# Optimization experiments

Hardware: AMD Instinct MI355X
Metric: run time of the kernel (lower is better)

## Reference

```python
import jax, jax.numpy as jnp
import numpy as np

N = 8192        # points
M = 131072      # query-key pairs (edges)
C_IN = 512
H = 8           # heads
D = 64          # head_channels
BINS = 48
BIN_SIZE = 0.05


def setup_inputs() -> dict:
    key = jax.random.key(0)
    ks = jax.random.split(key, 8)
    x_F = jax.random.normal(ks[0], (N, C_IN), dtype=jnp.float32)
    x_C = jax.random.uniform(ks[1], (N, 3), dtype=jnp.float32)
    qk_pair_idxs = jax.random.randint(ks[2], (2, M), 0, N, dtype=jnp.int64)
    W_qkv = jax.random.normal(ks[3], (C_IN, 3 * H * D), dtype=jnp.float32) * 0.02
    b_qkv = jnp.zeros((3 * H * D,), dtype=jnp.float32)
    q_tables = jax.random.normal(ks[4], (3, BINS, H, D), dtype=jnp.float32) * 0.02
    k_tables = jax.random.normal(ks[5], (3, BINS, H, D), dtype=jnp.float32) * 0.02
    v_tables = jax.random.normal(ks[6], (3, BINS, H, D), dtype=jnp.float32) * 0.02
    return {"x_F": x_F, "x_C": x_C, "qk_pair_idxs": qk_pair_idxs,
            "W_qkv": W_qkv, "b_qkv": b_qkv,
            "q_tables": q_tables, "k_tables": k_tables, "v_tables": v_tables}


def reference(x_F, x_C, qk_pair_idxs, W_qkv, b_qkv, q_tables, k_tables, v_tables):
    n = x_F.shape[0]
    qkv = (x_F @ W_qkv + b_qkv).reshape(n, 3, H, D)
    q = qkv[:, 0] * (D ** -0.5)   # scale folded into queries, as in the module
    k = qkv[:, 1]
    v = qkv[:, 2]
    qi = qk_pair_idxs[0]
    ki = qk_pair_idxs[1]
    # quantized relative coordinates -> table bin indices [M,3]
    rel = (x_C[qi] - x_C[ki]) / BIN_SIZE + BINS / 2
    idx = jnp.clip(rel.astype(jnp.int32), 0, BINS - 1)
    # precompute per-point, per-axis, per-bin table dot products [N,3,BINS,H]
    q_dot = jnp.einsum('nhd,abhd->nabh', q, q_tables)
    k_dot = jnp.einsum('nhd,abhd->nabh', k, k_tables)
    # content logits [M,H]
    logits = jnp.einsum('mhd,mhd->mh', q[qi], k[ki])
    for a in range(3):  # fixed xyz axes
        logits = logits + q_dot[qi, a, idx[:, a]] + k_dot[ki, a, idx[:, a]]
    # scatter softmax over query index (per head)
    seg_max = jax.ops.segment_max(logits, qi, num_segments=n)
    e = jnp.exp(logits - seg_max[qi])
    denom = jax.ops.segment_sum(e, qi, num_segments=n)
    attn = e / denom[qi]  # [M,H]
    # value-side relative position bias, summed over axes [M,H,D]
    vt = v_tables[0, idx[:, 0]] + v_tables[1, idx[:, 1]] + v_tables[2, idx[:, 2]]
    contrib = attn[:, :, None] * (v[ki] + vt)            # [M,H,D]
    agg = jax.ops.segment_sum(contrib, qi, num_segments=n)  # [N,H,D]
    return agg.reshape(n, H * D)
```

## Files before the change

### kernel.cpp

```cpp
#include <hip/hip_runtime.h>
#include <hip/hip_bf16.h>
#include <stdint.h>

#define N_PTS 8192
#define M_EDGES 131072
#define CIN 512
#define QKV_COLS 1536

typedef __bf16 bf16x8 __attribute__((ext_vector_type(8)));
typedef float f32x4 __attribute__((ext_vector_type(4)));

#define GAS __attribute__((address_space(1)))
#define LAS __attribute__((address_space(3)))

__device__ __forceinline__ void gload_lds16(const void* g, void* l) {
  __builtin_amdgcn_global_load_lds((const GAS void*)g, (LAS void*)l, 16, 0, 0);
}

__global__ __launch_bounds__(256) void prep_kernel(
    const float* __restrict__ xF, const float* __restrict__ W,
    const float* __restrict__ qt, const float* __restrict__ kt,
    const float* __restrict__ vt, const int* __restrict__ pairs,
    const float* __restrict__ xc,
    __bf16* __restrict__ A, __bf16* __restrict__ BT,
    __bf16* __restrict__ qtb, __bf16* __restrict__ ktb, __bf16* __restrict__ vtb,
    int* __restrict__ qi_a, unsigned* __restrict__ pack0, int* __restrict__ cnt) {
  __shared__ float tile[32][33];
  int b = blockIdx.x;
  int tid = threadIdx.x;
  if (b < 4096) {
    int base = (b * 256 + tid) * 4;
    float4 v = *(const float4*)(xF + base);
    A[base + 0] = (__bf16)v.x;
    A[base + 1] = (__bf16)v.y;
    A[base + 2] = (__bf16)v.z;
    A[base + 3] = (__bf16)v.w;
  } else if (b < 4864) {
    int blk = b - 4096;
    int bk = blk & 15, bn = blk >> 4;
    int x = tid & 31, y = tid >> 5;
#pragma unroll
    for (int j = 0; j < 4; j++) {
      int r = y + j * 8;
      tile[r][x] = W[(size_t)(bk * 32 + r) * QKV_COLS + bn * 32 + x];
    }
    __syncthreads();
#pragma unroll
    for (int j = 0; j < 4; j++) {
      int r = y + j * 8;
      BT[(size_t)(bn * 32 + r) * CIN + bk * 32 + x] = (__bf16)tile[x][r];
    }
  } else if (b < 5152) {
    int i = (b - 4864) * 256 + tid;
    int d = i & 63, h = (i >> 6) & 7, ab = i >> 9;
    int po = (h * 144 + ab) * 64 + d;
    qtb[po] = (__bf16)qt[i];
    ktb[po] = (__bf16)kt[i];
    vtb[i] = (__bf16)vt[i];
  } else {
    int m = (b - 5152) * 256 + tid;
    int qi = pairs[m], ki = pairs[M_EDGES + m];
    unsigned pb = 0;
#pragma unroll
    for (int a = 0; a < 3; a++) {
      float rel = (xc[qi * 3 + a] - xc[ki * 3 + a]) / 0.05f + 24.0f;
      int bb = (int)rel;
      bb = bb < 0 ? 0 : (bb > 47 ? 47 : bb);
      pb |= (unsigned)bb << (6 * a);
    }
    qi_a[m] = qi;
    pack0[m] = (unsigned)ki | (pb << 13);
    atomicAdd(&cnt[qi], 1);
  }
}

__global__ __launch_bounds__(256) void gemm_qkv(const __bf16* __restrict__ A,
                                                const __bf16* __restrict__ BT,
                                                const float* __restrict__ bias,
                                                __bf16* __restrict__ qb,
                                                __bf16* __restrict__ kb,
                                                __bf16* __restrict__ vb) {
  __shared__ __align__(16) char At[128 * 128];
  __shared__ __align__(16) char Bt[128 * 128];
  int tid = threadIdx.x;
  int w = tid >> 6, l = tid & 63;
  int bm = blockIdx.x, bn = blockIdx.y;
  int wm = w & 1, wn = w >> 1;
  f32x4 acc[4][4] = {};
  const char* Ab = (const char*)A;
  const char* Bb = (const char*)BT;
  int lr = l & 15;
  int lk = (l >> 4) * 16;
  int xr = (lr & 7) << 4;

  for (int kt = 0; kt < 8; kt++) {
#pragma unroll
    for (int r = 0; r < 4; r++) {
      int flat = r * 4096 + tid * 16;
      int row = flat >> 7, colb = flat & 127;
      int gcolb = colb ^ ((row & 7) << 4);
      gload_lds16(Ab + ((size_t)(bm * 128 + row) * CIN + kt * 64) * 2 + gcolb,
                  At + r * 4096 + w * 1024);
      gload_lds16(Bb + ((size_t)(bn * 128 + row) * CIN + kt * 64) * 2 + gcolb,
                  Bt + r * 4096 + w * 1024);
    }
    __syncthreads();
#pragma unroll
    for (int ks = 0; ks < 2; ks++) {
      bf16x8 af[4], bfr[4];
      int cs = (ks * 64 + lk) ^ xr;
#pragma unroll
      for (int mf = 0; mf < 4; mf++) af[mf] = *(const bf16x8*)(At + (wm * 64 + mf * 16 + lr) * 128 + cs);
#pragma unroll
      for (int nf = 0; nf < 4; nf++) bfr[nf] = *(const bf16x8*)(Bt + (wn * 64 + nf * 16 + lr) * 128 + cs);
#pragma unroll
      for (int mf = 0; mf < 4; mf++)
#pragma unroll
        for (int nf = 0; nf < 4; nf++)
          acc[mf][nf] = __builtin_amdgcn_mfma_f32_16x16x32_bf16(af[mf], bfr[nf], acc[mf][nf], 0, 0, 0);
    }
    __syncthreads();
  }

  int lg = l >> 4;
#pragma unroll
  for (int mf = 0; mf < 4; mf++) {
#pragma unroll
    for (int nf = 0; nf < 4; nf++) {
      int gc = bn * 128 + wn * 64 + nf * 16 + lr;
      float b = bias[gc];
      int which = gc >> 9;
      int col = gc & 511;
      __bf16* dst = which == 0 ? qb : (which == 1 ? kb : vb);
      float scale = which == 0 ? 0.125f : 1.0f;
#pragma unroll
      for (int j = 0; j < 4; j++) {
        int gr = bm * 128 + wm * 64 + mf * 16 + lg * 4 + j;
        dst[(size_t)gr * 512 + col] = (__bf16)((acc[mf][nf][j] + b) * scale);
      }
    }
  }
}

__global__ __launch_bounds__(256) void table_dot(const __bf16* __restrict__ qb,
                                                 const __bf16* __restrict__ kb,
                                                 const __bf16* __restrict__ qtb,
                                                 const __bf16* __restrict__ ktb,
                                                 __bf16* __restrict__ qdot,
                                                 __bf16* __restrict__ kdot) {
  __shared__ __align__(16) char As[128 * 128];
  __shared__ __align__(16) char Bs[144 * 128];
  int nt = blockIdx.x, h = blockIdx.y, z = blockIdx.z;
  const __bf16* src = z ? kb : qb;
  const __bf16* tab = z ? ktb : qtb;
  __bf16* out = z ? kdot : qdot;
  int tid = threadIdx.x, w = tid >> 6, l = tid & 63;
  const char* sb = (const char*)src;
  const char* tb = (const char*)tab + (size_t)h * 144 * 128;
#pragma unroll
  for (int p = 0; p < 4; p++) {
    int flat = p * 4096 + tid * 16;
    int row = flat >> 7, colb = flat & 127;
    int gcolb = colb ^ ((row & 7) << 4);
    gload_lds16(sb + (size_t)(nt * 128 + row) * 1024 + h * 128 + gcolb, As + p * 4096 + w * 1024);
    gload_lds16(tb + row * 128 + gcolb, Bs + p * 4096 + w * 1024);
  }
  if (w < 2) {
    int flat = 16384 + w * 1024 + l * 16;
    int row = flat >> 7, colb = flat & 127;
    int gcolb = colb ^ ((row & 7) << 4);
    gload_lds16(tb + row * 128 + gcolb, Bs + 16384 + w * 1024);
  }
  __syncthreads();

  f32x4 acc[2][9] = {};
  int lr = l & 15, lk = (l >> 4) * 16;
  int xr = (lr & 7) << 4;
#pragma unroll
  for (int ks = 0; ks < 2; ks++) {
    bf16x8 af[2], bf[9];
    int cs = (ks * 64 + lk) ^ xr;
#pragma unroll
    for (int mf = 0; mf < 2; mf++)
      af[mf] = *(const bf16x8*)(As + (w * 32 + mf * 16 + lr) * 128 + cs);
#pragma unroll
    for (int nf = 0; nf < 9; nf++)
      bf[nf] = *(const bf16x8*)(Bs + (nf * 16 + lr) * 128 + cs);
#pragma unroll
    for (int mf = 0; mf < 2; mf++)
#pragma unroll
      for (int nf = 0; nf < 9; nf++)
        acc[mf][nf] = __builtin_amdgcn_mfma_f32_16x16x32_bf16(af[mf], bf[nf], acc[mf][nf], 0, 0, 0);
  }

  int lg = l >> 4;
#pragma unroll
  for (int mf = 0; mf < 2; mf++)
#pragma unroll
    for (int nf = 0; nf < 9; nf++)
#pragma unroll
      for (int j = 0; j < 4; j++) {
        int n = nt * 128 + w * 32 + mf * 16 + lg * 4 + j;
        int ab = nf * 16 + lr;
        out[(size_t)n * 1152 + ab * 8 + h] = (__bf16)acc[mf][nf][j];
      }
}

__global__ __launch_bounds__(256) void scan_kernel(const int* __restrict__ cnt,
                                                   int* __restrict__ off,
                                                   int* __restrict__ cursor) {
  __shared__ int wsum[4];
  int tid = threadIdx.x, lane = tid & 63, w = tid >> 6;
  int local[32];
  int s = 0;
#pragma unroll
  for (int i = 0; i < 8; i++) {
    int4 v = ((const int4*)cnt)[tid * 8 + i];
    local[i * 4 + 0] = v.x; local[i * 4 + 1] = v.y;
    local[i * 4 + 2] = v.z; local[i * 4 + 3] = v.w;
    s += v.x + v.y + v.z + v.w;
  }
  int incl = s;
#pragma unroll
  for (int d = 1; d < 64; d <<= 1) {
    int t = __shfl_up(incl, d, 64);
    if (lane >= d) incl += t;
  }
  if (lane == 63) wsum[w] = incl;
  __syncthreads();
  int woff = 0;
#pragma unroll
  for (int j = 0; j < 4; j++) woff += (j < w) ? wsum[j] : 0;
  int run = woff + incl - s;
  int base = tid * 32;
#pragma unroll
  for (int i = 0; i < 32; i++) {
    off[base + i] = run;
    cursor[base + i] = run;
    run += local[i];
  }
  if (tid == 255) off[N_PTS] = run;
}

__global__ void scatter_k(const int* __restrict__ qi_a, const unsigned* __restrict__ pack0,
                          int* __restrict__ cursor, int* __restrict__ qi_s,
                          unsigned* __restrict__ epack) {
  int m = blockIdx.x * blockDim.x + threadIdx.x;
  if (m < M_EDGES) {
    int qi = qi_a[m];
    int pos = atomicAdd(&cursor[qi], 1);
    qi_s[pos] = qi;
    epack[pos] = pack0[m];
  }
}

__global__ void edge_bias(const int* __restrict__ qi_s, const unsigned* __restrict__ epack,
                          const __bf16* __restrict__ qdot, const __bf16* __restrict__ kdot,
                          float* __restrict__ eb) {
  int t = blockIdx.x * 256 + threadIdx.x;
  int e = t >> 3, h = t & 7;
  unsigned pk = epack[e];
  int ki = pk & 8191;
  unsigned pb = pk >> 13;
  int qi = qi_s[e];
  int a0 = ((int)(pb & 63)) * 8 + h;
  int a1 = (48 + (int)((pb >> 6) & 63)) * 8 + h;
  int a2 = (96 + (int)((pb >> 12) & 63)) * 8 + h;
  const __bf16* qd = qdot + qi * 1152;
  const __bf16* kd = kdot + ki * 1152;
  eb[t] = (float)qd[a0] + (float)qd[a1] + (float)qd[a2] +
          (float)kd[a0] + (float)kd[a1] + (float)kd[a2];
}

__global__ __launch_bounds__(512) void attn_kernel(
    const __bf16* __restrict__ qb, const __bf16* __restrict__ kb,
    const __bf16* __restrict__ vb, const __bf16* __restrict__ vtb,
    const float* __restrict__ eb, const int* __restrict__ off,
    const unsigned* __restrict__ epack, float* __restrict__ out) {
  int n = blockIdx.x;
  int tid = threadIdx.x;
  int h = tid >> 6, l = tid & 63;
  int es = l >> 3, dg = l & 7;
  int tcol = h * 64 + dg * 8;

  bf16x8 q8 = *(const bf16x8*)(qb + (n << 9) + tcol);
  float qv[8];
#pragma unroll
  for (int j = 0; j < 8; j++) qv[j] = (float)q8[j];

  float acc[8] = {0.f, 0.f, 0.f, 0.f, 0.f, 0.f, 0.f, 0.f};
  float den = 0.f;
  int e0 = off[n], e1 = off[n + 1];

  for (int base = e0; base < e1; base += 16) {
    int eA = base + es;
    int eB = base + 8 + es;
    int cA = eA < e1 ? eA : e1 - 1;
    int cB = eB < e1 ? eB : e1 - 1;
    unsigned pA = epack[cA], pB = epack[cB];
    float ebA = eb[(cA << 3) + h], ebB = eb[(cB << 3) + h];
    int kiA = pA & 8191, kiB = pB & 8191;
    unsigned bA = pA >> 13, bB = pB >> 13;
    bf16x8 kA8 = *(const bf16x8*)(kb + (kiA << 9) + tcol);
    bf16x8 vA8 = *(const bf16x8*)(vb + (kiA << 9) + tcol);
    bf16x8 kB8 = *(const bf16x8*)(kb + (kiB << 9) + tcol);
    bf16x8 vB8 = *(const bf16x8*)(vb + (kiB << 9) + tcol);
    bf16x8 tA0 = *(const bf16x8*)(vtb + ((bA & 63u) << 9) + tcol);
    bf16x8 tA1 = *(const bf16x8*)(vtb + ((48 + ((bA >> 6) & 63u)) << 9) + tcol);
    bf16x8 tA2 = *(const bf16x8*)(vtb + ((96 + ((bA >> 12) & 63u)) << 9) + tcol);
    bf16x8 tB0 = *(const bf16x8*)(vtb + ((bB & 63u) << 9) + tcol);
    bf16x8 tB1 = *(const bf16x8*)(vtb + ((48 + ((bB >> 6) & 63u)) << 9) + tcol);
    bf16x8 tB2 = *(const bf16x8*)(vtb + ((96 + ((bB >> 12) & 63u)) << 9) + tcol);
    float p1 = 0.f, p2 = 0.f;
#pragma unroll
    for (int j = 0; j < 8; j++) {
      p1 += qv[j] * (float)kA8[j];
      p2 += qv[j] * (float)kB8[j];
    }
    p1 += __shfl_xor(p1, 1, 64);
    p2 += __shfl_xor(p2, 1, 64);
    p1 += __shfl_xor(p1, 2, 64);
    p2 += __shfl_xor(p2, 2, 64);
    p1 += __shfl_xor(p1, 4, 64);
    p2 += __shfl_xor(p2, 4, 64);
    p1 += ebA;
    p2 += ebB;
    float x1 = (eA < e1) ? __expf(p1) : 0.f;
    float x2 = (eB < e1) ? __expf(p2) : 0.f;
    den += x1 + x2;
#pragma unroll
    for (int j = 0; j < 8; j++)
      acc[j] += x1 * ((float)vA8[j] + (float)tA0[j] + (float)tA1[j] + (float)tA2[j]) +
                x2 * ((float)vB8[j] + (float)tB0[j] + (float)tB1[j] + (float)tB2[j]);
  }

#pragma unroll
  for (int s = 8; s <= 32; s <<= 1) {
    den += __shfl_xor(den, s, 64);
#pragma unroll
    for (int j = 0; j < 8; j++) acc[j] += __shfl_xor(acc[j], s, 64);
  }

  if (l < 8) {
    float inv = (e1 > e0) ? 1.f / den : 0.f;
    float* op = out + (n << 9) + h * 64 + l * 8;
    f32x4 o0 = {acc[0] * inv, acc[1] * inv, acc[2] * inv, acc[3] * inv};
    f32x4 o1 = {acc[4] * inv, acc[5] * inv, acc[6] * inv, acc[7] * inv};
    *(f32x4*)op = o0;
    *(f32x4*)(op + 4) = o1;
  }
}

extern "C" void kernel_launch(void* const* d_in, const int* in_sizes, int n_in,
                              void* d_out, int out_size, void* d_ws, size_t ws_size,
                              hipStream_t stream) {
  const float* xF = (const float*)d_in[0];
  const float* xC = (const float*)d_in[1];
  const int* pairs = (const int*)d_in[2];
  const float* W = (const float*)d_in[3];
  const float* bias = (const float*)d_in[4];
  const float* qt = (const float*)d_in[5];
  const float* kt = (const float*)d_in[6];
  const float* vt = (const float*)d_in[7];
  float* out = (float*)d_out;

  char* ws = (char*)d_ws;
  size_t o = 0;
  auto alloc = [&](size_t bytes) {
    void* p = ws + o;
    o = (o + bytes + 255) & ~(size_t)255;
    return p;
  };
  __bf16* A = (__bf16*)alloc((size_t)N_PTS * CIN * 2);
  __bf16* BT = (__bf16*)alloc((size_t)QKV_COLS * CIN * 2);
  __bf16* qb = (__bf16*)alloc((size_t)N_PTS * 512 * 2);
  __bf16* kb = (__bf16*)alloc((size_t)N_PTS * 512 * 2);
  __bf16* vb = (__bf16*)alloc((size_t)N_PTS * 512 * 2);
  __bf16* qtb = (__bf16*)alloc((size_t)8 * 144 * 64 * 2);
  __bf16* ktb = (__bf16*)alloc((size_t)8 * 144 * 64 * 2);
  __bf16* vtb = (__bf16*)alloc((size_t)144 * 512 * 2);
  __bf16* qdot = (__bf16*)alloc((size_t)N_PTS * 1152 * 2);
  __bf16* kdot = (__bf16*)alloc((size_t)N_PTS * 1152 * 2);
  float* eb = (float*)alloc((size_t)M_EDGES * 8 * 4);
  int* qi_a = (int*)alloc(M_EDGES * 4);
  unsigned* pack0 = (unsigned*)alloc(M_EDGES * 4);
  int* qi_s = (int*)alloc(M_EDGES * 4);
  unsigned* epack = (unsigned*)alloc(M_EDGES * 4);
  int* cnt = (int*)alloc(N_PTS * 4);
  int* off = (int*)alloc((N_PTS + 1) * 4);
  int* cursor = (int*)alloc(N_PTS * 4);

  hipMemsetAsync(cnt, 0, N_PTS * 4, stream);

  prep_kernel<<<5664, 256, 0, stream>>>(xF, W, qt, kt, vt, pairs, xC,
                                        A, BT, qtb, ktb, vtb, qi_a, pack0, cnt);
  scan_kernel<<<1, 256, 0, stream>>>(cnt, off, cursor);
  scatter_k<<<M_EDGES / 256, 256, 0, stream>>>(qi_a, pack0, cursor, qi_s, epack);
  gemm_qkv<<<dim3(N_PTS / 128, QKV_COLS / 128), 256, 0, stream>>>(A, BT, bias, qb, kb, vb);
  table_dot<<<dim3(N_PTS / 128, 8, 2), 256, 0, stream>>>(qb, kb, qtb, ktb, qdot, kdot);
  edge_bias<<<(M_EDGES * 8) / 256, 256, 0, stream>>>(qi_s, epack, qdot, kdot, eb);
  attn_kernel<<<N_PTS, 512, 0, stream>>>(qb, kb, vb, vtb, eb, off, epack, out);
}
```

Measured before the change: 169.5 us.

## Replace per-edge value-table gathers with per-query bin histograms and MFMA finish

The attention kernel no longer gathers three value-table rows per edge. It accumulates softmax weights into a per-query, per-head histogram over the 144 bins using LDS atomics, writes unnormalized numerators, denominators and a bf16 histogram, and a new MFMA finish kernel multiplies the histograms by a transposed value table and normalizes. This cuts per-edge memory traffic and halves the loop width, at the cost of LDS atomics, an extra kernel, extra global round trips, and bf16 rounding of the histogram weights. The QKV GEMM M-tile is also halved to 64 to launch more blocks, and the histogram buffer reuses the GEMM input workspace.

```diff
diff --git a/kernel.cpp b/kernel.cpp
--- a/kernel.cpp
+++ b/kernel.cpp
@@ -23,7 +23,7 @@
     const float* __restrict__ vt, const int* __restrict__ pairs,
     const float* __restrict__ xc,
     __bf16* __restrict__ A, __bf16* __restrict__ BT,
-    __bf16* __restrict__ qtb, __bf16* __restrict__ ktb, __bf16* __restrict__ vtb,
+    __bf16* __restrict__ qtb, __bf16* __restrict__ ktb, __bf16* __restrict__ vtT,
     int* __restrict__ qi_a, unsigned* __restrict__ pack0, int* __restrict__ cnt) {
   __shared__ float tile[32][33];
   int b = blockIdx.x;
@@ -56,9 +56,14 @@
     int po = (h * 144 + ab) * 64 + d;
     qtb[po] = (__bf16)qt[i];
     ktb[po] = (__bf16)kt[i];
-    vtb[i] = (__bf16)vt[i];
+  } else if (b < 5472) {
+    int i = (b - 5152) * 256 + tid;
+    int p = i % 160;
+    int d = (i / 160) & 63;
+    int h = i / 10240;
+    vtT[i] = (p < 144) ? (__bf16)vt[p * 512 + h * 64 + d] : (__bf16)0.f;
   } else {
-    int m = (b - 5152) * 256 + tid;
+    int m = (b - 5472) * 256 + tid;
     int qi = pairs[m], ki = pairs[M_EDGES + m];
     unsigned pb = 0;
 #pragma unroll
@@ -80,13 +85,13 @@
                                                 __bf16* __restrict__ qb,
                                                 __bf16* __restrict__ kb,
                                                 __bf16* __restrict__ vb) {
-  __shared__ __align__(16) char At[128 * 128];
+  __shared__ __align__(16) char At[64 * 128];
   __shared__ __align__(16) char Bt[128 * 128];
   int tid = threadIdx.x;
   int w = tid >> 6, l = tid & 63;
   int bm = blockIdx.x, bn = blockIdx.y;
   int wm = w & 1, wn = w >> 1;
-  f32x4 acc[4][4] = {};
+  f32x4 acc[2][4] = {};
   const char* Ab = (const char*)A;
   const char* Bb = (const char*)BT;
   int lr = l & 15;
@@ -95,26 +100,32 @@
 
   for (int kt = 0; kt < 8; kt++) {
 #pragma unroll
+    for (int r = 0; r < 2; r++) {
+      int flat = r * 4096 + tid * 16;
+      int row = flat >> 7, colb = flat & 127;
+      int gcolb = colb ^ ((row & 7) << 4);
+      gload_lds16(Ab + ((size_t)(bm * 64 + row) * CIN + kt * 64) * 2 + gcolb,
+                  At + r * 4096 + w * 1024);
+    }
+#pragma unroll
     for (int r = 0; r < 4; r++) {
       int flat = r * 4096 + tid * 16;
       int row = flat >> 7, colb = flat & 127;
       int gcolb = colb ^ ((row & 7) << 4);
-      gload_lds16(Ab + ((size_t)(bm * 128 + row) * CIN + kt * 64) * 2 + gcolb,
-                  At + r * 4096 + w * 1024);
       gload_lds16(Bb + ((size_t)(bn * 128 + row) * CIN + kt * 64) * 2 + gcolb,
                   Bt + r * 4096 + w * 1024);
     }
     __syncthreads();
 #pragma unroll
     for (int ks = 0; ks < 2; ks++) {
-      bf16x8 af[4], bfr[4];
+      bf16x8 af[2], bfr[4];
       int cs = (ks * 64 + lk) ^ xr;
 #pragma unroll
-      for (int mf = 0; mf < 4; mf++) af[mf] = *(const bf16x8*)(At + (wm * 64 + mf * 16 + lr) * 128 + cs);
+      for (int mf = 0; mf < 2; mf++) af[mf] = *(const bf16x8*)(At + (wm * 32 + mf * 16 + lr) * 128 + cs);
 #pragma unroll
       for (int nf = 0; nf < 4; nf++) bfr[nf] = *(const bf16x8*)(Bt + (wn * 64 + nf * 16 + lr) * 128 + cs);
 #pragma unroll
-      for (int mf = 0; mf < 4; mf++)
+      for (int mf = 0; mf < 2; mf++)
 #pragma unroll
         for (int nf = 0; nf < 4; nf++)
           acc[mf][nf] = __builtin_amdgcn_mfma_f32_16x16x32_bf16(af[mf], bfr[nf], acc[mf][nf], 0, 0, 0);
@@ -124,7 +135,7 @@
 
   int lg = l >> 4;
 #pragma unroll
-  for (int mf = 0; mf < 4; mf++) {
+  for (int mf = 0; mf < 2; mf++) {
 #pragma unroll
     for (int nf = 0; nf < 4; nf++) {
       int gc = bn * 128 + wn * 64 + nf * 16 + lr;
@@ -135,7 +146,7 @@
       float scale = which == 0 ? 0.125f : 1.0f;
 #pragma unroll
       for (int j = 0; j < 4; j++) {
-        int gr = bm * 128 + wm * 64 + mf * 16 + lg * 4 + j;
+        int gr = bm * 64 + wm * 32 + mf * 16 + lg * 4 + j;
         dst[(size_t)gr * 512 + col] = (__bf16)((acc[mf][nf][j] + b) * scale);
       }
     }
@@ -274,80 +285,135 @@
 
 __global__ __launch_bounds__(512) void attn_kernel(
     const __bf16* __restrict__ qb, const __bf16* __restrict__ kb,
-    const __bf16* __restrict__ vb, const __bf16* __restrict__ vtb,
-    const float* __restrict__ eb, const int* __restrict__ off,
-    const unsigned* __restrict__ epack, float* __restrict__ out) {
+    const __bf16* __restrict__ vb, const float* __restrict__ eb,
+    const int* __restrict__ off, const unsigned* __restrict__ epack,
+    float* __restrict__ num, float* __restrict__ den, __bf16* __restrict__ Hb) {
+  __shared__ float hist[8 * 160];
   int n = blockIdx.x;
   int tid = threadIdx.x;
   int h = tid >> 6, l = tid & 63;
   int es = l >> 3, dg = l & 7;
   int tcol = h * 64 + dg * 8;
 
+  for (int i = tid; i < 1280; i += 512) hist[i] = 0.f;
+  __syncthreads();
+
   bf16x8 q8 = *(const bf16x8*)(qb + (n << 9) + tcol);
   float qv[8];
 #pragma unroll
   for (int j = 0; j < 8; j++) qv[j] = (float)q8[j];
 
   float acc[8] = {0.f, 0.f, 0.f, 0.f, 0.f, 0.f, 0.f, 0.f};
-  float den = 0.f;
+  float dn = 0.f;
   int e0 = off[n], e1 = off[n + 1];
 
-  for (int base = e0; base < e1; base += 16) {
-    int eA = base + es;
-    int eB = base + 8 + es;
-    int cA = eA < e1 ? eA : e1 - 1;
-    int cB = eB < e1 ? eB : e1 - 1;
-    unsigned pA = epack[cA], pB = epack[cB];
-    float ebA = eb[(cA << 3) + h], ebB = eb[(cB << 3) + h];
-    int kiA = pA & 8191, kiB = pB & 8191;
-    unsigned bA = pA >> 13, bB = pB >> 13;
-    bf16x8 kA8 = *(const bf16x8*)(kb + (kiA << 9) + tcol);
-    bf16x8 vA8 = *(const bf16x8*)(vb + (kiA << 9) + tcol);
-    bf16x8 kB8 = *(const bf16x8*)(kb + (kiB << 9) + tcol);
-    bf16x8 vB8 = *(const bf16x8*)(vb + (kiB << 9) + tcol);
-    bf16x8 tA0 = *(const bf16x8*)(vtb + ((bA & 63u) << 9) + tcol);
-    bf16x8 tA1 = *(const bf16x8*)(vtb + ((48 + ((bA >> 6) & 63u)) << 9) + tcol);
-    bf16x8 tA2 = *(const bf16x8*)(vtb + ((96 + ((bA >> 12) & 63u)) << 9) + tcol);
-    bf16x8 tB0 = *(const bf16x8*)(vtb + ((bB & 63u) << 9) + tcol);
-    bf16x8 tB1 = *(const bf16x8*)(vtb + ((48 + ((bB >> 6) & 63u)) << 9) + tcol);
-    bf16x8 tB2 = *(const bf16x8*)(vtb + ((96 + ((bB >> 12) & 63u)) << 9) + tcol);
-    float p1 = 0.f, p2 = 0.f;
-#pragma unroll
-    for (int j = 0; j < 8; j++) {
-      p1 += qv[j] * (float)kA8[j];
-      p2 += qv[j] * (float)kB8[j];
-    }
-    p1 += __shfl_xor(p1, 1, 64);
-    p2 += __shfl_xor(p2, 1, 64);
-    p1 += __shfl_xor(p1, 2, 64);
-    p2 += __shfl_xor(p2, 2, 64);
-    p1 += __shfl_xor(p1, 4, 64);
-    p2 += __shfl_xor(p2, 4, 64);
-    p1 += ebA;
-    p2 += ebB;
-    float x1 = (eA < e1) ? __expf(p1) : 0.f;
-    float x2 = (eB < e1) ? __expf(p2) : 0.f;
-    den += x1 + x2;
-#pragma unroll
-    for (int j = 0; j < 8; j++)
-      acc[j] += x1 * ((float)vA8[j] + (float)tA0[j] + (float)tA1[j] + (float)tA2[j]) +
-                x2 * ((float)vB8[j] + (float)tB0[j] + (float)tB1[j] + (float)tB2[j]);
+  for (int base = e0; base < e1; base += 8) {
+    int e = base + es;
+    bool valid = e < e1;
+    int ee = valid ? e : e0;
+    unsigned pk = epack[ee];
+    float ebv = eb[(ee << 3) + h];
+    int ki = pk & 8191;
+    unsigned pb = pk >> 13;
+    bf16x8 k8 = *(const bf16x8*)(kb + (ki << 9) + tcol);
+    bf16x8 v8 = *(const bf16x8*)(vb + (ki << 9) + tcol);
+    float p = 0.f;
+#pragma unroll
+    for (int j = 0; j < 8; j++) p += qv[j] * (float)k8[j];
+    p += __shfl_xor(p, 1, 64);
+    p += __shfl_xor(p, 2, 64);
+    p += __shfl_xor(p, 4, 64);
+    p += ebv;
+    float x = valid ? __expf(p) : 0.f;
+    dn += x;
+#pragma unroll
+    for (int j = 0; j < 8; j++) acc[j] += x * (float)v8[j];
+    if (dg == 0 && valid) {
+      float* hh = hist + h * 160;
+      atomicAdd(hh + (pb & 63), x);
+      atomicAdd(hh + 48 + ((pb >> 6) & 63), x);
+      atomicAdd(hh + 96 + ((pb >> 12) & 63), x);
+    }
   }
 
 #pragma unroll
   for (int s = 8; s <= 32; s <<= 1) {
-    den += __shfl_xor(den, s, 64);
+    dn += __shfl_xor(dn, s, 64);
 #pragma unroll
     for (int j = 0; j < 8; j++) acc[j] += __shfl_xor(acc[j], s, 64);
   }
 
   if (l < 8) {
-    float inv = (e1 > e0) ? 1.f / den : 0.f;
-    float* op = out + (n << 9) + h * 64 + l * 8;
-    f32x4 o0 = {acc[0] * inv, acc[1] * inv, acc[2] * inv, acc[3] * inv};
-    f32x4 o1 = {acc[4] * inv, acc[5] * inv, acc[6] * inv, acc[7] * inv};
+    float* op = num + (n << 9) + h * 64 + l * 8;
+    f32x4 o0 = {acc[0], acc[1], acc[2], acc[3]};
+    f32x4 o1 = {acc[4], acc[5], acc[6], acc[7]};
     *(f32x4*)op = o0;
     *(f32x4*)(op + 4) = o1;
+  }
+  if (l == 0) den[n * 8 + h] = dn;
+  __syncthreads();
+  for (int i = tid; i < 1280; i += 512) Hb[(size_t)n * 1280 + i] = (__bf16)hist[i];
+}
+
+__global__ __launch_bounds__(256) void finish_kernel(const __bf16* __restrict__ Hb,
+                                                     const __bf16* __restrict__ vtT,
+                                                     const float* __restrict__ den,
+                                                     float* __restrict__ out) {
+  __shared__ __align__(16) char As[128 * 64];
+  __shared__ __align__(16) char Bs[64 * 64];
+  int nt = blockIdx.x, h = blockIdx.y;
+  int tid = threadIdx.x, w = tid >> 6, l = tid & 63;
+  int lr = l & 15, lk = (l >> 4) * 16;
+  int xr = (lr & 3) << 4;
+  const char* Ab = (const char*)Hb;
+  const char* Bb = (const char*)vtT;
+  f32x4 acc[2][4] = {};
+
+  for (int kt = 0; kt < 5; kt++) {
+#pragma unroll
+    for (int c = 0; c < 2; c++) {
+      int flat = c * 4096 + tid * 16;
+      int row = flat >> 6, colb = flat & 63;
+      int gcolb = colb ^ ((row & 3) << 4);
+      gload_lds16(Ab + ((size_t)(nt * 128 + row) * 1280 + h * 160 + kt * 32) * 2 + gcolb,
+                  As + c * 4096 + w * 1024);
+    }
+    {
+      int flat = tid * 16;
+      int row = flat >> 6, colb = flat & 63;
+      int gcolb = colb ^ ((row & 3) << 4);
+      gload_lds16(Bb + ((size_t)(h * 64 + row) * 160 + kt * 32) * 2 + gcolb,
+                  Bs + w * 1024);
+    }
+    __syncthreads();
+    bf16x8 af[2], bf[4];
+    int cs = lk ^ xr;
+#pragma unroll
+    for (int mf = 0; mf < 2; mf++) af[mf] = *(const bf16x8*)(As + (w * 32 + mf * 16 + lr) * 64 + cs);
+#pragma unroll
+    for (int nf = 0; nf < 4; nf++) bf[nf] = *(const bf16x8*)(Bs + (nf * 16 + lr) * 64 + cs);
+#pragma unroll
+    for (int mf = 0; mf < 2; mf++)
+#pragma unroll
+      for (int nf = 0; nf < 4; nf++)
+        acc[mf][nf] = __builtin_amdgcn_mfma_f32_16x16x32_bf16(af[mf], bf[nf], acc[mf][nf], 0, 0, 0);
+    __syncthreads();
+  }
+
+  int lg = l >> 4;
+#pragma unroll
+  for (int mf = 0; mf < 2; mf++) {
+#pragma unroll
+    for (int j = 0; j < 4; j++) {
+      int n = nt * 128 + w * 32 + mf * 16 + lg * 4 + j;
+      float dnv = den[n * 8 + h];
+      float inv = dnv > 0.f ? 1.f / dnv : 0.f;
+#pragma unroll
+      for (int nf = 0; nf < 4; nf++) {
+        int gi = (n << 9) + h * 64 + nf * 16 + lr;
+        out[gi] = (out[gi] + acc[mf][nf][j]) * inv;
+      }
+    }
   }
 }
 
@@ -371,17 +437,20 @@
     o = (o + bytes + 255) & ~(size_t)255;
     return p;
   };
-  __bf16* A = (__bf16*)alloc((size_t)N_PTS * CIN * 2);
-  __bf16* BT = (__bf16*)alloc((size_t)QKV_COLS * CIN * 2);
+  char* region0 = (char*)alloc((size_t)N_PTS * 1280 * 2);
+  __bf16* A = (__bf16*)region0;
+  __bf16* BT = (__bf16*)(region0 + (size_t)N_PTS * CIN * 2);
+  __bf16* Hb = (__bf16*)region0;
   __bf16* qb = (__bf16*)alloc((size_t)N_PTS * 512 * 2);
   __bf16* kb = (__bf16*)alloc((size_t)N_PTS * 512 * 2);
   __bf16* vb = (__bf16*)alloc((size_t)N_PTS * 512 * 2);
   __bf16* qtb = (__bf16*)alloc((size_t)8 * 144 * 64 * 2);
   __bf16* ktb = (__bf16*)alloc((size_t)8 * 144 * 64 * 2);
-  __bf16* vtb = (__bf16*)alloc((size_t)144 * 512 * 2);
+  __bf16* vtT = (__bf16*)alloc((size_t)8 * 64 * 160 * 2);
   __bf16* qdot = (__bf16*)alloc((size_t)N_PTS * 1152 * 2);
   __bf16* kdot = (__bf16*)alloc((size_t)N_PTS * 1152 * 2);
   float* eb = (float*)alloc((size_t)M_EDGES * 8 * 4);
+  float* den = (float*)alloc((size_t)N_PTS * 8 * 4);
   int* qi_a = (int*)alloc(M_EDGES * 4);
   unsigned* pack0 = (unsigned*)alloc(M_EDGES * 4);
   int* qi_s = (int*)alloc(M_EDGES * 4);
@@ -392,12 +461,13 @@
 
   hipMemsetAsync(cnt, 0, N_PTS * 4, stream);
 
-  prep_kernel<<<5664, 256, 0, stream>>>(xF, W, qt, kt, vt, pairs, xC,
-                                        A, BT, qtb, ktb, vtb, qi_a, pack0, cnt);
+  prep_kernel<<<5984, 256, 0, stream>>>(xF, W, qt, kt, vt, pairs, xC,
+                                        A, BT, qtb, ktb, vtT, qi_a, pack0, cnt);
   scan_kernel<<<1, 256, 0, stream>>>(cnt, off, cursor);
   scatter_k<<<M_EDGES / 256, 256, 0, stream>>>(qi_a, pack0, cursor, qi_s, epack);
-  gemm_qkv<<<dim3(N_PTS / 128, QKV_COLS / 128), 256, 0, stream>>>(A, BT, bias, qb, kb, vb);
+  gemm_qkv<<<dim3(N_PTS / 64, QKV_COLS / 128), 256, 0, stream>>>(A, BT, bias, qb, kb, vb);
   table_dot<<<dim3(N_PTS / 128, 8, 2), 256, 0, stream>>>(qb, kb, qtb, ktb, qdot, kdot);
   edge_bias<<<(M_EDGES * 8) / 256, 256, 0, stream>>>(qi_s, epack, qdot, kdot, eb);
-  attn_kernel<<<N_PTS, 512, 0, stream>>>(qb, kb, vb, vtb, eb, off, epack, out);
-}
+  attn_kernel<<<N_PTS, 512, 0, stream>>>(qb, kb, vb, eb, off, epack, out, den, Hb);
+  finish_kernel<<<dim3(N_PTS / 128, 8), 256, 0, stream>>>(Hb, vtT, den, out);
+}
```

Result: no change. 171.9 us (+1.4%).
